# Kernel optimization log

Hardware: AMD Instinct MI355X
Metric: run time of the kernel (lower is better)

Reference implementation:

```python
import jax, jax.numpy as jnp
import numpy as np

BS, NE, NN, CIN, H, D = 8, 4800, 4981, 3, 128, 6
EPG = 19200
NEDGE = BS * EPG
N = BS * NE

PARAM_NAMES = [
    'enc_cw1','enc_cb1','enc_cw2','enc_cb2','enc_cw3','enc_clng','enc_clnb',
    'enc_ew1','enc_eb1','enc_ew2','enc_eb2','enc_ew3','enc_elng','enc_elnb',
    'p_ew1','p_eb1','p_ew2','p_eb2','p_ew3','p_elng','p_elnb',
    'p_nw1','p_nb1','p_nw2','p_nb2','p_nw3','p_nlng','p_nlnb',
    'dec_uw1','dec_ub1','dec_uw2','dec_ub2','dec_uw3','dec_ulng','dec_ulnb',
    'dec_cw1','dec_cb1','dec_cw2','dec_cb2','dec_cw3']


def setup_inputs():
    key = jax.random.key(0)
    ks = iter(jax.random.split(key, 64))
    def nrm(shape, s=0.1):
        return jax.random.normal(next(ks), shape, jnp.float32) * s
    inp = {}
    inp['x'] = jax.random.normal(next(ks), (BS * NN, CIN), jnp.float32)
    inp['elem_conn'] = jax.random.randint(next(ks), (NE, 4), 0, NN)
    inp['edge_index'] = jax.random.randint(next(ks), (2, NEDGE), 0, N)
    inp['enc_cw1'] = nrm((CIN, 4, 1)); inp['enc_cb1'] = nrm((CIN, 1), 0.01)
    inp['enc_cw2'] = nrm((CIN, 1, 1)); inp['enc_cb2'] = nrm((CIN, 1), 0.01)
    inp['enc_cw3'] = nrm((CIN, 1, 1))
    inp['enc_clng'] = jnp.ones((CIN, 1)); inp['enc_clnb'] = jnp.zeros((CIN, 1))
    inp['enc_ew1'] = nrm((CIN, H)); inp['enc_eb1'] = nrm((H,), 0.01)
    inp['enc_ew2'] = nrm((H, H)); inp['enc_eb2'] = nrm((H,), 0.01)
    inp['enc_ew3'] = nrm((H, H))
    inp['enc_elng'] = jnp.ones((H,)); inp['enc_elnb'] = jnp.zeros((H,))
    inp['p_ew1'] = nrm((D, 2 * H, H)); inp['p_eb1'] = nrm((D, H), 0.01)
    inp['p_ew2'] = nrm((D, H, H)); inp['p_eb2'] = nrm((D, H), 0.01)
    inp['p_ew3'] = nrm((D, H, H))
    inp['p_elng'] = jnp.ones((D, H)); inp['p_elnb'] = jnp.zeros((D, H))
    inp['p_nw1'] = nrm((D, 2 * H, H)); inp['p_nb1'] = nrm((D, H), 0.01)
    inp['p_nw2'] = nrm((D, H, H)); inp['p_nb2'] = nrm((D, H), 0.01)
    inp['p_nw3'] = nrm((D, H, H))
    inp['p_nlng'] = jnp.ones((D, H)); inp['p_nlnb'] = jnp.zeros((D, H))
    inp['dec_uw1'] = nrm((H, 1, 4)); inp['dec_ub1'] = nrm((H, 4), 0.01)
    inp['dec_uw2'] = nrm((H, 4, 4)); inp['dec_ub2'] = nrm((H, 4), 0.01)
    inp['dec_uw3'] = nrm((H, 4, 4))
    inp['dec_ulng'] = jnp.ones((H, 4)); inp['dec_ulnb'] = jnp.zeros((H, 4))
    inp['dec_cw1'] = nrm((H, CIN)); inp['dec_cb1'] = nrm((CIN,), 0.01)
    inp['dec_cw2'] = nrm((CIN, CIN)); inp['dec_cb2'] = nrm((CIN,), 0.01)
    inp['dec_cw3'] = nrm((CIN, CIN))
    return inp


def lrelu(x):
    return jnp.where(x >= 0, x, 0.2 * x)


def ln(x, g, b, axis=-1):
    m = jnp.mean(x, axis=axis, keepdims=True)
    v = jnp.var(x, axis=axis, keepdims=True)
    return (x - m) / jnp.sqrt(v + 1e-5) * g + b


def mlp(x, w1, b1, w2, b2, w3):
    h = lrelu(x @ w1 + b1)
    h = lrelu(h @ w2 + b2)
    return h @ w3


def _forward(fl, elem_conn, edge_index):
    x = fl[0]
    P = dict(zip(PARAM_NAMES, fl[1:]))
    # ---- Encoder: MeshCNN gather (4 mesh nodes per element) + per-channel MLP 4->1 ----
    xg = x.reshape(BS, NN, CIN)[:, elem_conn]                  # (BS, NE, 4, CIN)
    h = lrelu(jnp.einsum('beic,cio->beoc', xg, P['enc_cw1']) + P['enc_cb1'].T[None, None])
    h = lrelu(jnp.einsum('beic,cio->beoc', h, P['enc_cw2']) + P['enc_cb2'].T[None, None])
    h = jnp.einsum('beic,cio->beoc', h, P['enc_cw3'])
    h = ln(h, P['enc_clng'].T[None, None], P['enc_clnb'].T[None, None], axis=2)  # LayerNorm(1)
    h = h[:, :, 0, :].reshape(N, CIN)
    h = ln(mlp(h, P['enc_ew1'], P['enc_eb1'], P['enc_ew2'], P['enc_eb2'], P['enc_ew3']),
           P['enc_elng'], P['enc_elnb'])                       # (N, H)
    # ---- Processor: D GraphNet blocks, edge MLP + scatter-add + node MLP ----
    src, dest = edge_index[0], edge_index[1]
    stacked = (P['p_ew1'], P['p_eb1'], P['p_ew2'], P['p_eb2'], P['p_ew3'], P['p_elng'], P['p_elnb'],
               P['p_nw1'], P['p_nb1'], P['p_nw2'], P['p_nb2'], P['p_nw3'], P['p_nlng'], P['p_nlnb'])
    def step(hc, p):
        ew1, eb1, ew2, eb2, ew3, eg, ebv, nw1, nb1, nw2, nb2, nw3, ng, nbv = p
        msg = jnp.concatenate([hc[dest], hc[src]], axis=-1)    # (NEDGE, 2H)
        m = ln(mlp(msg, ew1, eb1, ew2, eb2, ew3), eg, ebv)
        aggr = jax.ops.segment_sum(m, dest, num_segments=N)
        hn = ln(mlp(jnp.concatenate([hc, aggr], axis=-1), nw1, nb1, nw2, nb2, nw3), ng, nbv)
        return hn, None
    h, _ = jax.lax.scan(step, h, stacked)
    # ---- Decoder: per-channel upsample 1->4 then index_add back to mesh nodes ----
    u = h.reshape(BS, NE, H)[:, :, None, :]                    # (BS, NE, 1, H)
    u = lrelu(jnp.einsum('beic,cio->beoc', u, P['dec_uw1']) + P['dec_ub1'].T[None, None])
    u = lrelu(jnp.einsum('beic,cio->beoc', u, P['dec_uw2']) + P['dec_ub2'].T[None, None])
    u = jnp.einsum('beic,cio->beoc', u, P['dec_uw3'])
    u = ln(u, P['dec_ulng'].T[None, None], P['dec_ulnb'].T[None, None], axis=2)  # (BS, NE, 4, H)
    out = jnp.zeros((BS, NN, H), u.dtype).at[:, elem_conn.reshape(-1)].add(u.reshape(BS, NE * 4, H))
    out = out.reshape(BS * NN, H)
    o = lrelu(out @ P['dec_cw1'] + P['dec_cb1'])
    o = lrelu(o @ P['dec_cw2'] + P['dec_cb2'])
    return o @ P['dec_cw3']


def reference(x, elem_conn, edge_index,
              enc_cw1, enc_cb1, enc_cw2, enc_cb2, enc_cw3, enc_clng, enc_clnb,
              enc_ew1, enc_eb1, enc_ew2, enc_eb2, enc_ew3, enc_elng, enc_elnb,
              p_ew1, p_eb1, p_ew2, p_eb2, p_ew3, p_elng, p_elnb,
              p_nw1, p_nb1, p_nw2, p_nb2, p_nw3, p_nlng, p_nlnb,
              dec_uw1, dec_ub1, dec_uw2, dec_ub2, dec_uw3, dec_ulng, dec_ulnb,
              dec_cw1, dec_cb1, dec_cw2, dec_cb2, dec_cw3):
    fl = (x, enc_cw1, enc_cb1, enc_cw2, enc_cb2, enc_cw3, enc_clng, enc_clnb,
          enc_ew1, enc_eb1, enc_ew2, enc_eb2, enc_ew3, enc_elng, enc_elnb,
          p_ew1, p_eb1, p_ew2, p_eb2, p_ew3, p_elng, p_elnb,
          p_nw1, p_nb1, p_nw2, p_nb2, p_nw3, p_nlng, p_nlnb,
          dec_uw1, dec_ub1, dec_uw2, dec_ub2, dec_uw3, dec_ulng, dec_ulnb,
          dec_cw1, dec_cb1, dec_cw2, dec_cb2, dec_cw3)
    return _forward(fl, elem_conn, edge_index)
```

## Files before the change

kernel.cpp:

```cpp
#include <hip/hip_runtime.h>
#include <hip/hip_fp16.h>
#include <math.h>

#define BS    8
#define NE    4800
#define NN    4981
#define CIN   3
#define HD    128
#define DBLK  6
#define NEDGE 153600
#define NTOT  38400
#define NMESH (BS*NN)
#define NNP   5120
#define EM    128

#define UW1T  0
#define UB1T  512
#define UW2T  1024
#define UB2T  3072
#define UW3T  3584
#define ULNGT 5632
#define ULNBT 6144
#define DWT_N 6656

typedef _Float16 f16;
typedef _Float16 f16x8 __attribute__((ext_vector_type(8)));
typedef float f32x4 __attribute__((ext_vector_type(4)));

__device__ __forceinline__ float lrelu(float x) { return x >= 0.0f ? x : 0.2f * x; }

__global__ __launch_bounds__(128)
void enc_const_kernel(const float* __restrict__ clnb,
                      const float* __restrict__ ew1, const float* __restrict__ eb1,
                      const float* __restrict__ ew2, const float* __restrict__ eb2,
                      const float* __restrict__ ew3,
                      const float* __restrict__ g, const float* __restrict__ b,
                      float* __restrict__ hv0) {
    __shared__ float s1[HD], s2[HD], s3[HD];
    int j = threadIdx.x;
    float a = eb1[j];
    for (int c = 0; c < CIN; ++c) a += clnb[c] * ew1[c * HD + j];
    s1[j] = lrelu(a);
    __syncthreads();
    a = eb2[j];
    for (int k = 0; k < HD; ++k) a += s1[k] * ew2[k * HD + j];
    s2[j] = lrelu(a);
    __syncthreads();
    a = 0.0f;
    for (int k = 0; k < HD; ++k) a += s2[k] * ew3[k * HD + j];
    s3[j] = a;
    __syncthreads();
    float m = 0.0f;
    for (int k = 0; k < HD; ++k) m += s3[k];
    m *= (1.0f / HD);
    float v = 0.0f;
    for (int k = 0; k < HD; ++k) { float d = s3[k] - m; v += d * d; }
    v *= (1.0f / HD);
    float rs = 1.0f / sqrtf(v + 1e-5f);
    hv0[j] = (s3[j] - m) * rs * g[j] + b[j];
}

__global__ __launch_bounds__(128)
void msg0_kernel(const float* __restrict__ hv0,
                 const float* __restrict__ ew1, const float* __restrict__ eb1,
                 const float* __restrict__ ew2, const float* __restrict__ eb2,
                 const float* __restrict__ ew3,
                 const float* __restrict__ g, const float* __restrict__ b,
                 float* __restrict__ m0) {
    __shared__ float s1[HD], s2[HD], s3[HD];
    int j = threadIdx.x;
    float a = eb1[j];
    for (int k = 0; k < HD; ++k) a += hv0[k] * (ew1[k * HD + j] + ew1[(k + HD) * HD + j]);
    s1[j] = lrelu(a);
    __syncthreads();
    a = eb2[j];
    for (int k = 0; k < HD; ++k) a += s1[k] * ew2[k * HD + j];
    s2[j] = lrelu(a);
    __syncthreads();
    a = 0.0f;
    for (int k = 0; k < HD; ++k) a += s2[k] * ew3[k * HD + j];
    s3[j] = a;
    __syncthreads();
    float m = 0.0f;
    for (int k = 0; k < HD; ++k) m += s3[k];
    m *= (1.0f / HD);
    float v = 0.0f;
    for (int k = 0; k < HD; ++k) { float d = s3[k] - m; v += d * d; }
    v *= (1.0f / HD);
    float rs = 1.0f / sqrtf(v + 1e-5f);
    m0[j] = (s3[j] - m) * rs * g[j] + b[j];
}

__global__ __launch_bounds__(256)
void init_h16_kernel(f16* __restrict__ h, const float* __restrict__ hv0, int n8) {
    __shared__ f16 v[HD];
    if (threadIdx.x < HD) v[threadIdx.x] = (f16)hv0[threadIdx.x];
    __syncthreads();
    for (int i = blockIdx.x * blockDim.x + threadIdx.x; i < n8; i += gridDim.x * blockDim.x)
        ((uint4*)h)[i] = ((const uint4*)v)[i & 15];
}

__global__ __launch_bounds__(256)
void conv_weights_kernel(const float* __restrict__ ew1, const float* __restrict__ ew2,
                         const float* __restrict__ ew3,
                         const float* __restrict__ nw1, const float* __restrict__ nw2,
                         const float* __restrict__ nw3, f16* __restrict__ wbuf) {
    int b = blockIdx.x;
    int d = b >> 3, m = b & 7;
    const float* src;
    switch (m) {
        case 0: src = ew1 + (size_t)d * 2 * HD * HD; break;
        case 1: src = ew1 + (size_t)d * 2 * HD * HD + HD * HD; break;
        case 2: src = ew2 + (size_t)d * HD * HD; break;
        case 3: src = ew3 + (size_t)d * HD * HD; break;
        case 4: src = nw1 + (size_t)d * 2 * HD * HD; break;
        case 5: src = nw1 + (size_t)d * 2 * HD * HD + HD * HD; break;
        case 6: src = nw2 + (size_t)d * HD * HD; break;
        default: src = nw3 + (size_t)d * HD * HD; break;
    }
    f16* out = wbuf + (size_t)b * HD * HD;
    for (int idx = threadIdx.x; idx < HD * HD; idx += 256) {
        int n = idx >> 7, k = idx & 127;
        out[idx] = (f16)src[k * HD + n];
    }
}

__global__ __launch_bounds__(256)
void conv_ebias_kernel(const float* __restrict__ eb1, f16* __restrict__ eb16) {
    for (int i = threadIdx.x; i < DBLK * HD; i += 256)
        eb16[i] = (f16)eb1[i];
}

__global__ __launch_bounds__(256)
void conv_dec_weights(const float* __restrict__ uw1, const float* __restrict__ ub1,
                      const float* __restrict__ uw2, const float* __restrict__ ub2,
                      const float* __restrict__ uw3, const float* __restrict__ ulng,
                      const float* __restrict__ ulnb, float* __restrict__ dwt) {
    int tid = threadIdx.x;
    for (int idx = tid; idx < 512; idx += 256) {
        int o = idx >> 7, c = idx & 127;
        dwt[UW1T + idx] = uw1[c * 4 + o];
        dwt[UB1T + idx] = ub1[c * 4 + o];
        dwt[UB2T + idx] = ub2[c * 4 + o];
        dwt[ULNGT + idx] = ulng[c * 4 + o];
        dwt[ULNBT + idx] = ulnb[c * 4 + o];
    }
    for (int idx = tid; idx < 2048; idx += 256) {
        int io = idx >> 7, c = idx & 127;
        dwt[UW2T + idx] = uw2[c * 16 + io];
        dwt[UW3T + idx] = uw3[c * 16 + io];
    }
}

__global__ __launch_bounds__(256)
void csr_hist(const int* __restrict__ key, int* __restrict__ deg, int n) {
    int e = blockIdx.x * 256 + threadIdx.x;
    if (e < n) atomicAdd(&deg[key[e]], 1);
}

__global__ __launch_bounds__(256)
void csr_scan1(const int* __restrict__ deg, int* __restrict__ rowptr,
               int* __restrict__ bsum) {
    __shared__ int s[256];
    int i = blockIdx.x * 256 + threadIdx.x;
    int v = deg[i];
    s[threadIdx.x] = v;
    __syncthreads();
    for (int off = 1; off < 256; off <<= 1) {
        int t = (threadIdx.x >= off) ? s[threadIdx.x - off] : 0;
        __syncthreads();
        s[threadIdx.x] += t;
        __syncthreads();
    }
    rowptr[i] = s[threadIdx.x] - v;
    if (threadIdx.x == 255) bsum[blockIdx.x] = s[255];
}

__global__ __launch_bounds__(256)
void csr_scan2(int* __restrict__ bsum, int nb) {
    __shared__ int s[256];
    int v = (threadIdx.x < nb) ? bsum[threadIdx.x] : 0;
    s[threadIdx.x] = v;
    __syncthreads();
    for (int off = 1; off < 256; off <<= 1) {
        int t = (threadIdx.x >= off) ? s[threadIdx.x - off] : 0;
        __syncthreads();
        s[threadIdx.x] += t;
        __syncthreads();
    }
    if (threadIdx.x < nb) bsum[threadIdx.x] = s[threadIdx.x] - v;
}

__global__ __launch_bounds__(256)
void csr_scan3(int* __restrict__ rowptr, const int* __restrict__ bsum) {
    int i = blockIdx.x * 256 + threadIdx.x;
    rowptr[i] += bsum[blockIdx.x];
}

__global__ __launch_bounds__(256)
void csr_scatter(const int* __restrict__ dest, const int* __restrict__ srcv,
                 const int* __restrict__ rowptr, int* __restrict__ cursor,
                 int* __restrict__ dsorted, int* __restrict__ ssorted) {
    int e = blockIdx.x * 256 + threadIdx.x;
    int d = dest[e];
    int pos = rowptr[d] + atomicAdd(&cursor[d], 1);
    dsorted[pos] = d;
    ssorted[pos] = srcv[e];
}

__global__ __launch_bounds__(256)
void mesh_scatter(const int* __restrict__ conn, const int* __restrict__ mrow,
                  int* __restrict__ mcur, int* __restrict__ mslot, int n) {
    int idx = blockIdx.x * 256 + threadIdx.x;
    if (idx < n) {
        int nd = conn[idx];
        int pos = mrow[nd] + atomicAdd(&mcur[nd], 1);
        mslot[pos] = idx;
    }
}

template <int NT>
__device__ __forceinline__ void stage_w(const f16* __restrict__ Wg, f16 (*Bt)[HD + 8],
                                        int tid) {
    #pragma unroll
    for (int t = 0; t < 2048 / NT; ++t) {
        int idx = tid + t * NT;
        int r = idx >> 4, c = (idx & 15) * 8;
        *(uint4*)(&Bt[r][c]) = *(const uint4*)(Wg + (size_t)r * HD + c);
    }
}

__device__ __forceinline__ void mfma_pass(const f16 (*A)[HD + 8], const f16 (*Bt)[HD + 8],
                                          int rt_base, int ct_base, int ln, int quad,
                                          f32x4 acc[2][4]) {
    #pragma unroll
    for (int ks = 0; ks < 4; ++ks) {
        int kb = ks * 32 + quad * 8;
        f16x8 a0 = *(const f16x8*)(&A[rt_base + ln][kb]);
        f16x8 a1 = *(const f16x8*)(&A[rt_base + 16 + ln][kb]);
        #pragma unroll
        for (int c = 0; c < 4; ++c) {
            f16x8 b = *(const f16x8*)(&Bt[ct_base + c * 16 + ln][kb]);
            acc[0][c] = __builtin_amdgcn_mfma_f32_16x16x32_f16(a0, b, acc[0][c], 0, 0, 0);
            acc[1][c] = __builtin_amdgcn_mfma_f32_16x16x32_f16(a1, b, acc[1][c], 0, 0, 0);
        }
    }
}

__global__ __launch_bounds__(512, 4)
void gn_edge(const f16* __restrict__ P1, const f16* __restrict__ P2,
             const int* __restrict__ dsorted, const int* __restrict__ ssorted,
             const f16* __restrict__ W2, const f16* __restrict__ W3,
             const f16* __restrict__ b1h, const float* __restrict__ b2,
             const float* __restrict__ g, const float* __restrict__ bln,
             f16* __restrict__ msg) {
    __shared__ __align__(16) f16 As[EM][HD + 8];
    __shared__ __align__(16) f16 Bt[HD][HD + 8];
    __shared__ float red[EM][2][2];
    __shared__ int dS[EM], sS[EM];

    const int tid = threadIdx.x;
    const int base = blockIdx.x * EM;
    const int wave = tid >> 6, lane = tid & 63;
    const int ln = lane & 15, quad = lane >> 4;
    const int rt_base = (wave >> 1) * 32;
    const int ct_base = (wave & 1) * 64;
    const int half = wave & 1;

    if (tid < EM) dS[tid] = dsorted[base + tid];
    else if (tid < 2 * EM) sS[tid - EM] = ssorted[base + tid - EM];
    __syncthreads();

    const f16 k02s = (f16)0.2f;
    const f16x8 k02 = {k02s, k02s, k02s, k02s, k02s, k02s, k02s, k02s};

    stage_w<512>(W2, Bt, tid);
    #pragma unroll
    for (int t = 0; t < 4; ++t) {
        int idx = tid + t * 512;
        int r = idx >> 4, c = (idx & 15) * 8;
        f16x8 p1 = *(const f16x8*)(P1 + (size_t)dS[r] * HD + c);
        f16x8 p2 = *(const f16x8*)(P2 + (size_t)sS[r] * HD + c);
        f16x8 bb = *(const f16x8*)(b1h + c);
        f16x8 s = p1 + p2 + bb;
        f16x8 o = __builtin_elementwise_max(s, s * k02);
        *(f16x8*)(&As[r][c]) = o;
    }
    __syncthreads();

    f32x4 acc[2][4];

    #pragma unroll
    for (int c = 0; c < 4; ++c) {
        float bj = b2[ct_base + c * 16 + ln];
        f32x4 bb = {bj, bj, bj, bj};
        acc[0][c] = bb; acc[1][c] = bb;
    }
    mfma_pass(As, Bt, rt_base, ct_base, ln, quad, acc);
    __syncthreads();
    stage_w<512>(W3, Bt, tid);
    #pragma unroll
    for (int i = 0; i < 2; ++i)
        #pragma unroll
        for (int c = 0; c < 4; ++c)
            #pragma unroll
            for (int r = 0; r < 4; ++r)
                As[rt_base + i * 16 + quad * 4 + r][ct_base + c * 16 + ln] =
                    (f16)lrelu(acc[i][c][r]);
    __syncthreads();

    #pragma unroll
    for (int c = 0; c < 4; ++c) { f32x4 z = {0,0,0,0}; acc[0][c] = z; acc[1][c] = z; }
    mfma_pass(As, Bt, rt_base, ct_base, ln, quad, acc);

    #pragma unroll
    for (int i = 0; i < 2; ++i)
        #pragma unroll
        for (int r = 0; r < 4; ++r) {
            float s = acc[i][0][r] + acc[i][1][r] + acc[i][2][r] + acc[i][3][r];
            float q = acc[i][0][r] * acc[i][0][r] + acc[i][1][r] * acc[i][1][r] +
                      acc[i][2][r] * acc[i][2][r] + acc[i][3][r] * acc[i][3][r];
            s += __shfl_xor(s, 1); q += __shfl_xor(q, 1);
            s += __shfl_xor(s, 2); q += __shfl_xor(q, 2);
            s += __shfl_xor(s, 4); q += __shfl_xor(q, 4);
            s += __shfl_xor(s, 8); q += __shfl_xor(q, 8);
            if (ln == 0) {
                int row = rt_base + i * 16 + quad * 4 + r;
                red[row][half][0] = s;
                red[row][half][1] = q;
            }
        }
    __syncthreads();

    float gv[4], bv[4];
    #pragma unroll
    for (int c = 0; c < 4; ++c) {
        int col = ct_base + c * 16 + ln;
        gv[c] = g[col]; bv[c] = bln[col];
    }
    #pragma unroll
    for (int i = 0; i < 2; ++i)
        #pragma unroll
        for (int r = 0; r < 4; ++r) {
            int row = rt_base + i * 16 + quad * 4 + r;
            float s = red[row][0][0] + red[row][1][0];
            float q = red[row][0][1] + red[row][1][1];
            float m = s * (1.0f / HD);
            float var = q * (1.0f / HD) - m * m;
            float rs = 1.0f / sqrtf(var + 1e-5f);
            #pragma unroll
            for (int c = 0; c < 4; ++c) {
                int col = ct_base + c * 16 + ln;
                float v = (acc[i][c][r] - m) * rs * gv[c] + bv[c];
                msg[(size_t)(base + row) * HD + col] = (f16)v;
            }
        }
}

template <int AGGR, bool PROD>
__global__ __launch_bounds__(256, 3)
void gn_node(f16* __restrict__ h16, const f16* __restrict__ msg,
             const int* __restrict__ rowptr, const int* __restrict__ deg,
             const float* __restrict__ m0,
             const f16* __restrict__ W1a, const f16* __restrict__ W1b,
             const f16* __restrict__ W2, const f16* __restrict__ W3,
             const float* __restrict__ b1, const float* __restrict__ b2,
             const float* __restrict__ g, const float* __restrict__ bln,
             const f16* __restrict__ nW1a, const f16* __restrict__ nW1b,
             f16* __restrict__ P1, f16* __restrict__ P2) {
    __shared__ __align__(16) f16 As[64][HD + 8];
    __shared__ __align__(16) f16 Bt[HD][HD + 8];
    __shared__ float red[64][2][2];
    int* rpS = (int*)&red[0][0][0];
    int* dgS = rpS + 64;

    const int tid = threadIdx.x;
    const int base = blockIdx.x * 64;
    const int wave = tid >> 6, lane = tid & 63;
    const int ln = lane & 15, quad = lane >> 4;
    const int rt_base = (wave >> 1) * 32;
    const int ct_base = (wave & 1) * 64;
    const int half = wave & 1;

    if (tid < 64) {
        if (AGGR == 1) rpS[tid] = rowptr[base + tid];
        dgS[tid] = deg[base + tid];
    }
    __syncthreads();

    f16x8 hreg[4];
    #pragma unroll
    for (int t = 0; t < 4; ++t) {
        int idx = tid + t * 256;
        int r = idx >> 4, c = (idx & 15) * 8;
        hreg[t] = *(const f16x8*)(h16 + (size_t)(base + r) * HD + c);
        if (AGGR == 0) {
            float sc = (float)dgS[r];
            f16x8 o;
            #pragma unroll
            for (int u = 0; u < 8; ++u) o[u] = (f16)(sc * m0[c + u]);
            *(f16x8*)(&As[r][c]) = o;
        } else {
            int rp = rpS[r], dg = dgS[r];
            float a[8] = {0, 0, 0, 0, 0, 0, 0, 0};
            for (int j = 0; j < dg; ++j) {
                f16x8 mv = *(const f16x8*)(msg + (size_t)(rp + j) * HD + c);
                #pragma unroll
                for (int u = 0; u < 8; ++u) a[u] += (float)mv[u];
            }
            f16x8 o;
            #pragma unroll
            for (int u = 0; u < 8; ++u) o[u] = (f16)a[u];
            *(f16x8*)(&As[r][c]) = o;
        }
    }
    stage_w<256>(W1b, Bt, tid);
    __syncthreads();

    f32x4 acc[2][4];
    #pragma unroll
    for (int c = 0; c < 4; ++c) {
        float bj = b1[ct_base + c * 16 + ln];
        f32x4 bb = {bj, bj, bj, bj};
        acc[0][c] = bb; acc[1][c] = bb;
    }
    mfma_pass(As, Bt, rt_base, ct_base, ln, quad, acc);
    __syncthreads();

    #pragma unroll
    for (int t = 0; t < 4; ++t) {
        int idx = tid + t * 256;
        int r = idx >> 4, c = (idx & 15) * 8;
        *(f16x8*)(&As[r][c]) = hreg[t];
    }
    stage_w<256>(W1a, Bt, tid);
    __syncthreads();
    mfma_pass(As, Bt, rt_base, ct_base, ln, quad, acc);
    __syncthreads();

    stage_w<256>(W2, Bt, tid);
    #pragma unroll
    for (int i = 0; i < 2; ++i)
        #pragma unroll
        for (int c = 0; c < 4; ++c)
            #pragma unroll
            for (int r = 0; r < 4; ++r)
                As[rt_base + i * 16 + quad * 4 + r][ct_base + c * 16 + ln] =
                    (f16)lrelu(acc[i][c][r]);
    __syncthreads();

    #pragma unroll
    for (int c = 0; c < 4; ++c) {
        float bj = b2[ct_base + c * 16 + ln];
        f32x4 bb = {bj, bj, bj, bj};
        acc[0][c] = bb; acc[1][c] = bb;
    }
    mfma_pass(As, Bt, rt_base, ct_base, ln, quad, acc);
    __syncthreads();
    stage_w<256>(W3, Bt, tid);
    #pragma unroll
    for (int i = 0; i < 2; ++i)
        #pragma unroll
        for (int c = 0; c < 4; ++c)
            #pragma unroll
            for (int r = 0; r < 4; ++r)
                As[rt_base + i * 16 + quad * 4 + r][ct_base + c * 16 + ln] =
                    (f16)lrelu(acc[i][c][r]);
    __syncthreads();

    #pragma unroll
    for (int c = 0; c < 4; ++c) { f32x4 z = {0,0,0,0}; acc[0][c] = z; acc[1][c] = z; }
    mfma_pass(As, Bt, rt_base, ct_base, ln, quad, acc);

    #pragma unroll
    for (int i = 0; i < 2; ++i)
        #pragma unroll
        for (int r = 0; r < 4; ++r) {
            float s = acc[i][0][r] + acc[i][1][r] + acc[i][2][r] + acc[i][3][r];
            float q = acc[i][0][r] * acc[i][0][r] + acc[i][1][r] * acc[i][1][r] +
                      acc[i][2][r] * acc[i][2][r] + acc[i][3][r] * acc[i][3][r];
            s += __shfl_xor(s, 1); q += __shfl_xor(q, 1);
            s += __shfl_xor(s, 2); q += __shfl_xor(q, 2);
            s += __shfl_xor(s, 4); q += __shfl_xor(q, 4);
            s += __shfl_xor(s, 8); q += __shfl_xor(q, 8);
            if (ln == 0) {
                int row = rt_base + i * 16 + quad * 4 + r;
                red[row][half][0] = s;
                red[row][half][1] = q;
            }
        }
    __syncthreads();

    float gv[4], bv[4];
    #pragma unroll
    for (int c = 0; c < 4; ++c) {
        int col = ct_base + c * 16 + ln;
        gv[c] = g[col]; bv[c] = bln[col];
    }
    #pragma unroll
    for (int i = 0; i < 2; ++i)
        #pragma unroll
        for (int r = 0; r < 4; ++r) {
            int row = rt_base + i * 16 + quad * 4 + r;
            float s = red[row][0][0] + red[row][1][0];
            float q = red[row][0][1] + red[row][1][1];
            float m = s * (1.0f / HD);
            float var = q * (1.0f / HD) - m * m;
            float rs = 1.0f / sqrtf(var + 1e-5f);
            #pragma unroll
            for (int c = 0; c < 4; ++c) {
                int col = ct_base + c * 16 + ln;
                float v = (acc[i][c][r] - m) * rs * gv[c] + bv[c];
                f16 hv = (f16)v;
                h16[(size_t)(base + row) * HD + col] = hv;
                if (PROD) As[row][col] = hv;
            }
        }

    if (PROD) {
        __syncthreads();
        stage_w<256>(nW1a, Bt, tid);
        __syncthreads();
        #pragma unroll
        for (int c = 0; c < 4; ++c) { f32x4 z = {0,0,0,0}; acc[0][c] = z; acc[1][c] = z; }
        mfma_pass(As, Bt, rt_base, ct_base, ln, quad, acc);
        #pragma unroll
        for (int i = 0; i < 2; ++i)
            #pragma unroll
            for (int c = 0; c < 4; ++c)
                #pragma unroll
                for (int r = 0; r < 4; ++r)
                    P1[(size_t)(base + rt_base + i * 16 + quad * 4 + r) * HD +
                       ct_base + c * 16 + ln] = (f16)acc[i][c][r];
        __syncthreads();
        stage_w<256>(nW1b, Bt, tid);
        __syncthreads();
        #pragma unroll
        for (int c = 0; c < 4; ++c) { f32x4 z = {0,0,0,0}; acc[0][c] = z; acc[1][c] = z; }
        mfma_pass(As, Bt, rt_base, ct_base, ln, quad, acc);
        #pragma unroll
        for (int i = 0; i < 2; ++i)
            #pragma unroll
            for (int c = 0; c < 4; ++c)
                #pragma unroll
                for (int r = 0; r < 4; ++r)
                    P2[(size_t)(base + rt_base + i * 16 + quad * 4 + r) * HD +
                       ct_base + c * 16 + ln] = (f16)acc[i][c][r];
    }
}

__global__ __launch_bounds__(256)
void dec_store_kernel(const f16* __restrict__ h, const float* __restrict__ dwt,
                      f16* __restrict__ uval) {
    __shared__ f16 ub[2][4][HD];
    int tid = threadIdx.x;
    int idx = blockIdx.x * 256 + tid;
    int c = idx & 127;
    int nl = tid >> 7;
    float s = (float)h[idx];
    float u1[4], u2[4], u3[4];
    #pragma unroll
    for (int o = 0; o < 4; ++o)
        u1[o] = lrelu(s * dwt[UW1T + o * 128 + c] + dwt[UB1T + o * 128 + c]);
    #pragma unroll
    for (int o = 0; o < 4; ++o) {
        float a = dwt[UB2T + o * 128 + c];
        #pragma unroll
        for (int i = 0; i < 4; ++i) a += u1[i] * dwt[UW2T + (i * 4 + o) * 128 + c];
        u2[o] = lrelu(a);
    }
    #pragma unroll
    for (int o = 0; o < 4; ++o) {
        float a = 0.f;
        #pragma unroll
        for (int i = 0; i < 4; ++i) a += u2[i] * dwt[UW3T + (i * 4 + o) * 128 + c];
        u3[o] = a;
    }
    float m = 0.25f * (u3[0] + u3[1] + u3[2] + u3[3]);
    float var = 0.f;
    #pragma unroll
    for (int o = 0; o < 4; ++o) { float d = u3[o] - m; var += d * d; }
    var *= 0.25f;
    float rs = 1.0f / sqrtf(var + 1e-5f);
    #pragma unroll
    for (int o = 0; o < 4; ++o) {
        float val = (u3[o] - m) * rs * dwt[ULNGT + o * 128 + c] + dwt[ULNBT + o * 128 + c];
        ub[nl][o][c] = (f16)val;
    }
    __syncthreads();
    int nl2 = tid >> 7, rem = tid & 127;
    uint2 v = ((const uint2*)&ub[nl2][0][0])[rem];
    ((uint2*)(uval + (size_t)(blockIdx.x * 2 + nl2) * 4 * HD))[rem] = v;
}

__global__ __launch_bounds__(256)
void dec_gather_out(const f16* __restrict__ uval,
                    const int* __restrict__ mrow, const int* __restrict__ mdeg,
                    const int* __restrict__ mslot,
                    const float* __restrict__ cw1, const float* __restrict__ cb1,
                    const float* __restrict__ cw2, const float* __restrict__ cb2,
                    const float* __restrict__ cw3,
                    float* __restrict__ o, int nrows) {
    int r = blockIdx.x * 4 + (threadIdx.x >> 6);
    if (r >= nrows) return;
    int lane = threadIdx.x & 63;
    int b = r / NN, n = r - b * NN;
    int rp = mrow[n], dg = mdeg[n];
    size_t boff = (size_t)b * NE * 4;
    float a0 = 0.f, a1 = 0.f;
    for (int j = 0; j < dg; ++j) {
        int slot = mslot[rp + j];
        const f16* up = uval + (boff + slot) * HD + lane * 2;
        a0 += (float)up[0];
        a1 += (float)up[1];
    }
    int c0 = lane * 2, c1 = lane * 2 + 1;
    float s[3];
    #pragma unroll
    for (int k = 0; k < 3; ++k)
        s[k] = a0 * cw1[c0 * 3 + k] + a1 * cw1[c1 * 3 + k];
    #pragma unroll
    for (int off = 32; off >= 1; off >>= 1) {
        s[0] += __shfl_down(s[0], off);
        s[1] += __shfl_down(s[1], off);
        s[2] += __shfl_down(s[2], off);
    }
    if (lane == 0) {
        float t1[3], t2[3];
        #pragma unroll
        for (int k = 0; k < 3; ++k) t1[k] = lrelu(s[k] + cb1[k]);
        #pragma unroll
        for (int k = 0; k < 3; ++k) {
            float a = cb2[k];
            #pragma unroll
            for (int q = 0; q < 3; ++q) a += t1[q] * cw2[q * 3 + k];
            t2[k] = lrelu(a);
        }
        #pragma unroll
        for (int k = 0; k < 3; ++k) {
            float a = 0.f;
            #pragma unroll
            for (int q = 0; q < 3; ++q) a += t2[q] * cw3[q * 3 + k];
            o[(size_t)r * 3 + k] = a;
        }
    }
}

extern "C" void kernel_launch(void* const* d_in, const int* in_sizes, int n_in,
                              void* d_out, int out_size, void* d_ws, size_t ws_size,
                              hipStream_t stream) {
    const int* elem_conn = (const int*)d_in[1];
    const int* edge_index = (const int*)d_in[2];
    const int* e_src = edge_index;
    const int* e_dst = edge_index + NEDGE;
    const float* enc_clnb = (const float*)d_in[9];
    const float* enc_ew1 = (const float*)d_in[10];
    const float* enc_eb1 = (const float*)d_in[11];
    const float* enc_ew2 = (const float*)d_in[12];
    const float* enc_eb2 = (const float*)d_in[13];
    const float* enc_ew3 = (const float*)d_in[14];
    const float* enc_elng = (const float*)d_in[15];
    const float* enc_elnb = (const float*)d_in[16];
    const float* p_ew1 = (const float*)d_in[17];
    const float* p_eb1 = (const float*)d_in[18];
    const float* p_ew2 = (const float*)d_in[19];
    const float* p_eb2 = (const float*)d_in[20];
    const float* p_ew3 = (const float*)d_in[21];
    const float* p_elng = (const float*)d_in[22];
    const float* p_elnb = (const float*)d_in[23];
    const float* p_nw1 = (const float*)d_in[24];
    const float* p_nb1 = (const float*)d_in[25];
    const float* p_nw2 = (const float*)d_in[26];
    const float* p_nb2 = (const float*)d_in[27];
    const float* p_nw3 = (const float*)d_in[28];
    const float* p_nlng = (const float*)d_in[29];
    const float* p_nlnb = (const float*)d_in[30];
    const float* dec_uw1 = (const float*)d_in[31];
    const float* dec_ub1 = (const float*)d_in[32];
    const float* dec_uw2 = (const float*)d_in[33];
    const float* dec_ub2 = (const float*)d_in[34];
    const float* dec_uw3 = (const float*)d_in[35];
    const float* dec_ulng = (const float*)d_in[36];
    const float* dec_ulnb = (const float*)d_in[37];
    const float* dec_cw1 = (const float*)d_in[38];
    const float* dec_cb1 = (const float*)d_in[39];
    const float* dec_cw2 = (const float*)d_in[40];
    const float* dec_cb2 = (const float*)d_in[41];
    const float* dec_cw3 = (const float*)d_in[42];

    char* ws = (char*)d_ws;
    f16*   h16     = (f16*)(ws);
    f16*   wbuf    = (f16*)(ws + 9830400);
    float* hv0     = (float*)(ws + 11403264);
    float* m0      = (float*)(ws + 11403776);
    f16*   P1      = (f16*)(ws + 11404288);
    f16*   P2      = (f16*)(ws + 21234688);
    f16*   msg     = (f16*)(ws + 31065088);
    f16*   uval    = (f16*)(ws + 31065088);
    int*   deg     = (int*)(ws + 70386688);
    int*   rowptr  = (int*)(ws + 70540288);
    int*   cursor  = (int*)(ws + 70693888);
    int*   bsum    = (int*)(ws + 70847488);
    int*   dsorted = (int*)(ws + 70848512);
    int*   ssorted = (int*)(ws + 71462912);
    int*   mdeg    = (int*)(ws + 70693888);
    int*   mrow    = (int*)(ws + 70714368);
    int*   mcur    = (int*)(ws + 70734848);
    int*   mbsum   = (int*)(ws + 70755328);
    int*   mslot   = (int*)(ws + 70756352);
    float* dwt     = (float*)P1;
    f16*   eb16    = (f16*)(ws + 72077312);

    enc_const_kernel<<<1, 128, 0, stream>>>(enc_clnb, enc_ew1, enc_eb1, enc_ew2,
                                            enc_eb2, enc_ew3, enc_elng, enc_elnb, hv0);
    init_h16_kernel<<<1200, 256, 0, stream>>>(h16, hv0, NTOT * HD / 8);
    conv_weights_kernel<<<48, 256, 0, stream>>>(p_ew1, p_ew2, p_ew3,
                                                p_nw1, p_nw2, p_nw3, wbuf);
    conv_ebias_kernel<<<1, 256, 0, stream>>>(p_eb1, eb16);
    msg0_kernel<<<1, 128, 0, stream>>>(hv0, p_ew1, p_eb1, p_ew2, p_eb2, p_ew3,
                                       p_elng, p_elnb, m0);

    hipMemsetAsync(deg, 0, NTOT * sizeof(int), stream);
    hipMemsetAsync(cursor, 0, NTOT * sizeof(int), stream);
    csr_hist<<<NEDGE / 256, 256, 0, stream>>>(e_dst, deg, NEDGE);
    csr_scan1<<<NTOT / 256, 256, 0, stream>>>(deg, rowptr, bsum);
    csr_scan2<<<1, 256, 0, stream>>>(bsum, NTOT / 256);
    csr_scan3<<<NTOT / 256, 256, 0, stream>>>(rowptr, bsum);
    csr_scatter<<<NEDGE / 256, 256, 0, stream>>>(e_dst, e_src, rowptr, cursor,
                                                 dsorted, ssorted);

    hipMemsetAsync(mdeg, 0, NNP * sizeof(int), stream);
    hipMemsetAsync(mcur, 0, NNP * sizeof(int), stream);
    csr_hist<<<(NE * 4 + 255) / 256, 256, 0, stream>>>(elem_conn, mdeg, NE * 4);
    csr_scan1<<<NNP / 256, 256, 0, stream>>>(mdeg, mrow, mbsum);
    csr_scan2<<<1, 256, 0, stream>>>(mbsum, NNP / 256);
    csr_scan3<<<NNP / 256, 256, 0, stream>>>(mrow, mbsum);
    mesh_scatter<<<(NE * 4 + 255) / 256, 256, 0, stream>>>(elem_conn, mrow, mcur,
                                                           mslot, NE * 4);

    {
        const f16* wd = wbuf;
        const f16* wn = wbuf + (size_t)8 * HD * HD;
        gn_node<0, true><<<NTOT / 64, 256, 0, stream>>>(
            h16, nullptr, nullptr, deg, m0,
            wd + 4 * HD * HD, wd + 5 * HD * HD, wd + 6 * HD * HD, wd + 7 * HD * HD,
            p_nb1, p_nb2, p_nlng, p_nlnb,
            wn + 0 * HD * HD, wn + 1 * HD * HD, P1, P2);
    }

    for (int d = 1; d < DBLK; ++d) {
        const f16* wd = wbuf + (size_t)d * 8 * HD * HD;
        gn_edge<<<NEDGE / EM, 512, 0, stream>>>(
            P1, P2, dsorted, ssorted,
            wd + 2 * HD * HD, wd + 3 * HD * HD,
            eb16 + (size_t)d * HD, p_eb2 + (size_t)d * HD,
            p_elng + (size_t)d * HD, p_elnb + (size_t)d * HD, msg);
        if (d < DBLK - 1) {
            const f16* wn = wbuf + (size_t)(d + 1) * 8 * HD * HD;
            gn_node<1, true><<<NTOT / 64, 256, 0, stream>>>(
                h16, msg, rowptr, deg, nullptr,
                wd + 4 * HD * HD, wd + 5 * HD * HD, wd + 6 * HD * HD, wd + 7 * HD * HD,
                p_nb1 + (size_t)d * HD, p_nb2 + (size_t)d * HD,
                p_nlng + (size_t)d * HD, p_nlnb + (size_t)d * HD,
                wn + 0 * HD * HD, wn + 1 * HD * HD, P1, P2);
        } else {
            gn_node<1, false><<<NTOT / 64, 256, 0, stream>>>(
                h16, msg, rowptr, deg, nullptr,
                wd + 4 * HD * HD, wd + 5 * HD * HD, wd + 6 * HD * HD, wd + 7 * HD * HD,
                p_nb1 + (size_t)d * HD, p_nb2 + (size_t)d * HD,
                p_nlng + (size_t)d * HD, p_nlnb + (size_t)d * HD,
                wbuf, wbuf, P1, P2);
        }
    }

    conv_dec_weights<<<1, 256, 0, stream>>>(dec_uw1, dec_ub1, dec_uw2, dec_ub2,
                                            dec_uw3, dec_ulng, dec_ulnb, dwt);
    dec_store_kernel<<<NTOT * HD / 256, 256, 0, stream>>>(h16, dwt, uval);
    dec_gather_out<<<(NMESH + 3) / 4, 256, 0, stream>>>(
        uval, mrow, mdeg, mslot, dec_cw1, dec_cb1, dec_cw2, dec_cb2, dec_cw3,
        (float*)d_out, NMESH);
}
```

Measured before the change: 640.5 us.

## Read MFMA weight operands directly from global memory instead of LDS staging

Result: slower. 848.9 us (+32.5%).

```diff
diff --git a/kernel.cpp b/kernel.cpp
--- a/kernel.cpp
+++ b/kernel.cpp
@@ -219,20 +219,10 @@
     }
 }
 
-template <int NT>
-__device__ __forceinline__ void stage_w(const f16* __restrict__ Wg, f16 (*Bt)[HD + 8],
-                                        int tid) {
-    #pragma unroll
-    for (int t = 0; t < 2048 / NT; ++t) {
-        int idx = tid + t * NT;
-        int r = idx >> 4, c = (idx & 15) * 8;
-        *(uint4*)(&Bt[r][c]) = *(const uint4*)(Wg + (size_t)r * HD + c);
-    }
-}
-
-__device__ __forceinline__ void mfma_pass(const f16 (*A)[HD + 8], const f16 (*Bt)[HD + 8],
+__device__ __forceinline__ void mfma_pass(const f16 (*A)[HD + 8], const f16* __restrict__ Bg,
                                           int rt_base, int ct_base, int ln, int quad,
                                           f32x4 acc[2][4]) {
+    const f16* bp = Bg + (size_t)(ct_base + ln) * HD + quad * 8;
     #pragma unroll
     for (int ks = 0; ks < 4; ++ks) {
         int kb = ks * 32 + quad * 8;
@@ -240,14 +230,14 @@
         f16x8 a1 = *(const f16x8*)(&A[rt_base + 16 + ln][kb]);
         #pragma unroll
         for (int c = 0; c < 4; ++c) {
-            f16x8 b = *(const f16x8*)(&Bt[ct_base + c * 16 + ln][kb]);
+            f16x8 b = *(const f16x8*)(bp + (size_t)c * 16 * HD + ks * 32);
             acc[0][c] = __builtin_amdgcn_mfma_f32_16x16x32_f16(a0, b, acc[0][c], 0, 0, 0);
             acc[1][c] = __builtin_amdgcn_mfma_f32_16x16x32_f16(a1, b, acc[1][c], 0, 0, 0);
         }
     }
 }
 
-__global__ __launch_bounds__(512, 4)
+__global__ __launch_bounds__(512, 6)
 void gn_edge(const f16* __restrict__ P1, const f16* __restrict__ P2,
              const int* __restrict__ dsorted, const int* __restrict__ ssorted,
              const f16* __restrict__ W2, const f16* __restrict__ W3,
@@ -255,7 +245,6 @@
              const float* __restrict__ g, const float* __restrict__ bln,
              f16* __restrict__ msg) {
     __shared__ __align__(16) f16 As[EM][HD + 8];
-    __shared__ __align__(16) f16 Bt[HD][HD + 8];
     __shared__ float red[EM][2][2];
     __shared__ int dS[EM], sS[EM];
 
@@ -274,7 +263,6 @@
     const f16 k02s = (f16)0.2f;
     const f16x8 k02 = {k02s, k02s, k02s, k02s, k02s, k02s, k02s, k02s};
 
-    stage_w<512>(W2, Bt, tid);
     #pragma unroll
     for (int t = 0; t < 4; ++t) {
         int idx = tid + t * 512;
@@ -296,9 +284,8 @@
         f32x4 bb = {bj, bj, bj, bj};
         acc[0][c] = bb; acc[1][c] = bb;
     }
-    mfma_pass(As, Bt, rt_base, ct_base, ln, quad, acc);
-    __syncthreads();
-    stage_w<512>(W3, Bt, tid);
+    mfma_pass(As, W2, rt_base, ct_base, ln, quad, acc);
+    __syncthreads();
     #pragma unroll
     for (int i = 0; i < 2; ++i)
         #pragma unroll
@@ -311,7 +298,7 @@
 
     #pragma unroll
     for (int c = 0; c < 4; ++c) { f32x4 z = {0,0,0,0}; acc[0][c] = z; acc[1][c] = z; }
-    mfma_pass(As, Bt, rt_base, ct_base, ln, quad, acc);
+    mfma_pass(As, W3, rt_base, ct_base, ln, quad, acc);
 
     #pragma unroll
     for (int i = 0; i < 2; ++i)
@@ -358,7 +345,7 @@
 }
 
 template <int AGGR, bool PROD>
-__global__ __launch_bounds__(256, 3)
+__global__ __launch_bounds__(256, 5)
 void gn_node(f16* __restrict__ h16, const f16* __restrict__ msg,
              const int* __restrict__ rowptr, const int* __restrict__ deg,
              const float* __restrict__ m0,
@@ -369,7 +356,6 @@
              const f16* __restrict__ nW1a, const f16* __restrict__ nW1b,
              f16* __restrict__ P1, f16* __restrict__ P2) {
     __shared__ __align__(16) f16 As[64][HD + 8];
-    __shared__ __align__(16) f16 Bt[HD][HD + 8];
     __shared__ float red[64][2][2];
     int* rpS = (int*)&red[0][0][0];
     int* dgS = rpS + 64;
@@ -414,7 +400,6 @@
             *(f16x8*)(&As[r][c]) = o;
         }
     }
-    stage_w<256>(W1b, Bt, tid);
     __syncthreads();
 
     f32x4 acc[2][4];
@@ -424,7 +409,7 @@
         f32x4 bb = {bj, bj, bj, bj};
         acc[0][c] = bb; acc[1][c] = bb;
     }
-    mfma_pass(As, Bt, rt_base, ct_base, ln, quad, acc);
+    mfma_pass(As, W1b, rt_base, ct_base, ln, quad, acc);
     __syncthreads();
 
     #pragma unroll
@@ -433,12 +418,10 @@
         int r = idx >> 4, c = (idx & 15) * 8;
         *(f16x8*)(&As[r][c]) = hreg[t];
     }
-    stage_w<256>(W1a, Bt, tid);
-    __syncthreads();
-    mfma_pass(As, Bt, rt_base, ct_base, ln, quad, acc);
-    __syncthreads();
-
-    stage_w<256>(W2, Bt, tid);
+    __syncthreads();
+    mfma_pass(As, W1a, rt_base, ct_base, ln, quad, acc);
+    __syncthreads();
+
     #pragma unroll
     for (int i = 0; i < 2; ++i)
         #pragma unroll
@@ -455,9 +438,8 @@
         f32x4 bb = {bj, bj, bj, bj};
         acc[0][c] = bb; acc[1][c] = bb;
     }
-    mfma_pass(As, Bt, rt_base, ct_base, ln, quad, acc);
-    __syncthreads();
-    stage_w<256>(W3, Bt, tid);
+    mfma_pass(As, W2, rt_base, ct_base, ln, quad, acc);
+    __syncthreads();
     #pragma unroll
     for (int i = 0; i < 2; ++i)
         #pragma unroll
@@ -470,7 +452,7 @@
 
     #pragma unroll
     for (int c = 0; c < 4; ++c) { f32x4 z = {0,0,0,0}; acc[0][c] = z; acc[1][c] = z; }
-    mfma_pass(As, Bt, rt_base, ct_base, ln, quad, acc);
+    mfma_pass(As, W3, rt_base, ct_base, ln, quad, acc);
 
     #pragma unroll
     for (int i = 0; i < 2; ++i)
@@ -519,11 +501,9 @@
 
     if (PROD) {
         __syncthreads();
-        stage_w<256>(nW1a, Bt, tid);
-        __syncthreads();
         #pragma unroll
         for (int c = 0; c < 4; ++c) { f32x4 z = {0,0,0,0}; acc[0][c] = z; acc[1][c] = z; }
-        mfma_pass(As, Bt, rt_base, ct_base, ln, quad, acc);
+        mfma_pass(As, nW1a, rt_base, ct_base, ln, quad, acc);
         #pragma unroll
         for (int i = 0; i < 2; ++i)
             #pragma unroll
@@ -532,12 +512,9 @@
                 for (int r = 0; r < 4; ++r)
                     P1[(size_t)(base + rt_base + i * 16 + quad * 4 + r) * HD +
                        ct_base + c * 16 + ln] = (f16)acc[i][c][r];
-        __syncthreads();
-        stage_w<256>(nW1b, Bt, tid);
-        __syncthreads();
         #pragma unroll
         for (int c = 0; c < 4; ++c) { f32x4 z = {0,0,0,0}; acc[0][c] = z; acc[1][c] = z; }
-        mfma_pass(As, Bt, rt_base, ct_base, ln, quad, acc);
+        mfma_pass(As, nW1b, rt_base, ct_base, ln, quad, acc);
         #pragma unroll
         for (int i = 0; i < 2; ++i)
             #pragma unroll
```

## Make gn_edge persistent with double-buffered gather and resident weights

Applied to the files above, without the earlier changes.

New measurement: 655.2 us. 2.3% more time.

```diff
diff --git a/kernel.cpp b/kernel.cpp
--- a/kernel.cpp
+++ b/kernel.cpp
@@ -13,6 +13,9 @@
 #define NMESH (BS*NN)
 #define NNP   5120
 #define EM    128
+#define NTILE (NEDGE / EM)
+#define EGRID 240
+#define TPB   (NTILE / EGRID)
 
 #define UW1T  0
 #define UB1T  512
@@ -247,114 +250,152 @@
     }
 }
 
-__global__ __launch_bounds__(512, 4)
+__global__ __launch_bounds__(512, 2)
 void gn_edge(const f16* __restrict__ P1, const f16* __restrict__ P2,
              const int* __restrict__ dsorted, const int* __restrict__ ssorted,
              const f16* __restrict__ W2, const f16* __restrict__ W3,
              const f16* __restrict__ b1h, const float* __restrict__ b2,
              const float* __restrict__ g, const float* __restrict__ bln,
              f16* __restrict__ msg) {
-    __shared__ __align__(16) f16 As[EM][HD + 8];
-    __shared__ __align__(16) f16 Bt[HD][HD + 8];
+    __shared__ __align__(16) f16 Ag[2][EM][HD + 8];
+    __shared__ __align__(16) f16 Bt2[HD][HD + 8];
+    __shared__ __align__(16) f16 Bt3[HD][HD + 8];
     __shared__ float red[EM][2][2];
-    __shared__ int dS[EM], sS[EM];
 
     const int tid = threadIdx.x;
-    const int base = blockIdx.x * EM;
     const int wave = tid >> 6, lane = tid & 63;
     const int ln = lane & 15, quad = lane >> 4;
     const int rt_base = (wave >> 1) * 32;
     const int ct_base = (wave & 1) * 64;
     const int half = wave & 1;
-
-    if (tid < EM) dS[tid] = dsorted[base + tid];
-    else if (tid < 2 * EM) sS[tid - EM] = ssorted[base + tid - EM];
-    __syncthreads();
+    const int r0 = tid >> 4;
+    const int cg = (tid & 15) * 8;
+
+    const int t0 = blockIdx.x * TPB;
+    const int t1 = t0 + TPB;
 
     const f16 k02s = (f16)0.2f;
     const f16x8 k02 = {k02s, k02s, k02s, k02s, k02s, k02s, k02s, k02s};
-
-    stage_w<512>(W2, Bt, tid);
-    #pragma unroll
-    for (int t = 0; t < 4; ++t) {
-        int idx = tid + t * 512;
-        int r = idx >> 4, c = (idx & 15) * 8;
-        f16x8 p1 = *(const f16x8*)(P1 + (size_t)dS[r] * HD + c);
-        f16x8 p2 = *(const f16x8*)(P2 + (size_t)sS[r] * HD + c);
-        f16x8 bb = *(const f16x8*)(b1h + c);
+    const f16x8 bb = *(const f16x8*)(b1h + cg);
+
+    int dI[4], sI[4];
+    #pragma unroll
+    for (int it = 0; it < 4; ++it) {
+        dI[it] = dsorted[t0 * EM + r0 + it * 32];
+        sI[it] = ssorted[t0 * EM + r0 + it * 32];
+    }
+    stage_w<512>(W2, Bt2, tid);
+    stage_w<512>(W3, Bt3, tid);
+    #pragma unroll
+    for (int it = 0; it < 4; ++it) {
+        f16x8 p1 = *(const f16x8*)(P1 + (size_t)dI[it] * HD + cg);
+        f16x8 p2 = *(const f16x8*)(P2 + (size_t)sI[it] * HD + cg);
         f16x8 s = p1 + p2 + bb;
-        f16x8 o = __builtin_elementwise_max(s, s * k02);
-        *(f16x8*)(&As[r][c]) = o;
-    }
-    __syncthreads();
-
-    f32x4 acc[2][4];
-
-    #pragma unroll
-    for (int c = 0; c < 4; ++c) {
-        float bj = b2[ct_base + c * 16 + ln];
-        f32x4 bb = {bj, bj, bj, bj};
-        acc[0][c] = bb; acc[1][c] = bb;
-    }
-    mfma_pass(As, Bt, rt_base, ct_base, ln, quad, acc);
-    __syncthreads();
-    stage_w<512>(W3, Bt, tid);
-    #pragma unroll
-    for (int i = 0; i < 2; ++i)
-        #pragma unroll
-        for (int c = 0; c < 4; ++c)
-            #pragma unroll
-            for (int r = 0; r < 4; ++r)
-                As[rt_base + i * 16 + quad * 4 + r][ct_base + c * 16 + ln] =
-                    (f16)lrelu(acc[i][c][r]);
-    __syncthreads();
-
-    #pragma unroll
-    for (int c = 0; c < 4; ++c) { f32x4 z = {0,0,0,0}; acc[0][c] = z; acc[1][c] = z; }
-    mfma_pass(As, Bt, rt_base, ct_base, ln, quad, acc);
-
-    #pragma unroll
-    for (int i = 0; i < 2; ++i)
-        #pragma unroll
-        for (int r = 0; r < 4; ++r) {
-            float s = acc[i][0][r] + acc[i][1][r] + acc[i][2][r] + acc[i][3][r];
-            float q = acc[i][0][r] * acc[i][0][r] + acc[i][1][r] * acc[i][1][r] +
-                      acc[i][2][r] * acc[i][2][r] + acc[i][3][r] * acc[i][3][r];
-            s += __shfl_xor(s, 1); q += __shfl_xor(q, 1);
-            s += __shfl_xor(s, 2); q += __shfl_xor(q, 2);
-            s += __shfl_xor(s, 4); q += __shfl_xor(q, 4);
-            s += __shfl_xor(s, 8); q += __shfl_xor(q, 8);
-            if (ln == 0) {
+        *(f16x8*)(&Ag[0][r0 + it * 32][cg]) = __builtin_elementwise_max(s, s * k02);
+    }
+    #pragma unroll
+    for (int it = 0; it < 4; ++it) {
+        dI[it] = dsorted[(t0 + 1) * EM + r0 + it * 32];
+        sI[it] = ssorted[(t0 + 1) * EM + r0 + it * 32];
+    }
+    __syncthreads();
+
+    int b = 0;
+    for (int t = t0; t < t1; ++t, b ^= 1) {
+        const int base = t * EM;
+        f32x4 acc[2][4];
+
+        #pragma unroll
+        for (int c = 0; c < 4; ++c) {
+            float bj = b2[ct_base + c * 16 + ln];
+            f32x4 bv = {bj, bj, bj, bj};
+            acc[0][c] = bv; acc[1][c] = bv;
+        }
+        mfma_pass(Ag[b], Bt2, rt_base, ct_base, ln, quad, acc);
+        __syncthreads();
+
+        const bool hasNext = (t + 1 < t1);
+        f16x8 q1[4], q2[4];
+        if (hasNext) {
+            #pragma unroll
+            for (int it = 0; it < 4; ++it) {
+                q1[it] = *(const f16x8*)(P1 + (size_t)dI[it] * HD + cg);
+                q2[it] = *(const f16x8*)(P2 + (size_t)sI[it] * HD + cg);
+            }
+        }
+        #pragma unroll
+        for (int i = 0; i < 2; ++i)
+            #pragma unroll
+            for (int c = 0; c < 4; ++c)
+                #pragma unroll
+                for (int r = 0; r < 4; ++r)
+                    Ag[b][rt_base + i * 16 + quad * 4 + r][ct_base + c * 16 + ln] =
+                        (f16)lrelu(acc[i][c][r]);
+        if (t + 2 < t1) {
+            #pragma unroll
+            for (int it = 0; it < 4; ++it) {
+                dI[it] = dsorted[(t + 2) * EM + r0 + it * 32];
+                sI[it] = ssorted[(t + 2) * EM + r0 + it * 32];
+            }
+        }
+        __syncthreads();
+
+        #pragma unroll
+        for (int c = 0; c < 4; ++c) { f32x4 z = {0,0,0,0}; acc[0][c] = z; acc[1][c] = z; }
+        mfma_pass(Ag[b], Bt3, rt_base, ct_base, ln, quad, acc);
+
+        #pragma unroll
+        for (int i = 0; i < 2; ++i)
+            #pragma unroll
+            for (int r = 0; r < 4; ++r) {
+                float s = acc[i][0][r] + acc[i][1][r] + acc[i][2][r] + acc[i][3][r];
+                float q = acc[i][0][r] * acc[i][0][r] + acc[i][1][r] * acc[i][1][r] +
+                          acc[i][2][r] * acc[i][2][r] + acc[i][3][r] * acc[i][3][r];
+                s += __shfl_xor(s, 1); q += __shfl_xor(q, 1);
+                s += __shfl_xor(s, 2); q += __shfl_xor(q, 2);
+                s += __shfl_xor(s, 4); q += __shfl_xor(q, 4);
+                s += __shfl_xor(s, 8); q += __shfl_xor(q, 8);
+                if (ln == 0) {
+                    int row = rt_base + i * 16 + quad * 4 + r;
+                    red[row][half][0] = s;
+                    red[row][half][1] = q;
+                }
+            }
+
+        if (hasNext) {
+            #pragma unroll
+            for (int it = 0; it < 4; ++it) {
+                f16x8 s = q1[it] + q2[it] + bb;
+                *(f16x8*)(&Ag[b ^ 1][r0 + it * 32][cg]) =
+                    __builtin_elementwise_max(s, s * k02);
+            }
+        }
+        __syncthreads();
+
+        float gv[4], bv[4];
+        #pragma unroll
+        for (int c = 0; c < 4; ++c) {
+            int col = ct_base + c * 16 + ln;
+            gv[c] = g[col]; bv[c] = bln[col];
+        }
+        #pragma unroll
+        for (int i = 0; i < 2; ++i)
+            #pragma unroll
+            for (int r = 0; r < 4; ++r) {
                 int row = rt_base + i * 16 + quad * 4 + r;
-                red[row][half][0] = s;
-                red[row][half][1] = q;
+                float s = red[row][0][0] + red[row][1][0];
+                float q = red[row][0][1] + red[row][1][1];
+                float m = s * (1.0f / HD);
+                float var = q * (1.0f / HD) - m * m;
+                float rs = 1.0f / sqrtf(var + 1e-5f);
+                #pragma unroll
+                for (int c = 0; c < 4; ++c) {
+                    int col = ct_base + c * 16 + ln;
+                    float v = (acc[i][c][r] - m) * rs * gv[c] + bv[c];
+                    msg[(size_t)(base + row) * HD + col] = (f16)v;
+                }
             }
-        }
-    __syncthreads();
-
-    float gv[4], bv[4];
-    #pragma unroll
-    for (int c = 0; c < 4; ++c) {
-        int col = ct_base + c * 16 + ln;
-        gv[c] = g[col]; bv[c] = bln[col];
-    }
-    #pragma unroll
-    for (int i = 0; i < 2; ++i)
-        #pragma unroll
-        for (int r = 0; r < 4; ++r) {
-            int row = rt_base + i * 16 + quad * 4 + r;
-            float s = red[row][0][0] + red[row][1][0];
-            float q = red[row][0][1] + red[row][1][1];
-            float m = s * (1.0f / HD);
-            float var = q * (1.0f / HD) - m * m;
-            float rs = 1.0f / sqrtf(var + 1e-5f);
-            #pragma unroll
-            for (int c = 0; c < 4; ++c) {
-                int col = ct_base + c * 16 + ln;
-                float v = (acc[i][c][r] - m) * rs * gv[c] + bv[c];
-                msg[(size_t)(base + row) * HD + col] = (f16)v;
-            }
-        }
+    }
 }
 
 template <int AGGR, bool PROD>
@@ -750,7 +791,7 @@
 
     for (int d = 1; d < DBLK; ++d) {
         const f16* wd = wbuf + (size_t)d * 8 * HD * HD;
-        gn_edge<<<NEDGE / EM, 512, 0, stream>>>(
+        gn_edge<<<EGRID, 512, 0, stream>>>(
             P1, P2, dsorted, ssorted,
             wd + 2 * HD * HD, wd + 3 * HD * HD,
             eb16 + (size_t)d * HD, p_eb2 + (size_t)d * HD,
```
